# Performance work log

Measured on AMD Instinct MI355X. Metric: run time of the kernel, lower is better.

## Reference

```python
import jax, jax.numpy as jnp
import numpy as np

N = 100000   # num_nodes
R = 8        # num_relations
D = 64       # hidden_dim
E = 3200000  # num_edges


def setup_inputs() -> dict:
    key = jax.random.key(0)
    ks = jax.random.split(key, 10)
    s = 1.0 / np.sqrt(D)
    return {
        "x": jnp.arange(N, dtype=jnp.int64),
        "edge_index": jax.random.randint(ks[0], (2, E), 0, N, dtype=jnp.int64),
        "edge_type": jax.random.randint(ks[1], (E,), 0, R, dtype=jnp.int64),
        "emb": jax.random.normal(ks[2], (N, D), dtype=jnp.float32),
        "W1": jax.random.normal(ks[3], (R, D, D), dtype=jnp.float32) * s,
        "root1": jax.random.normal(ks[4], (D, D), dtype=jnp.float32) * s,
        "b1": jnp.zeros((D,), dtype=jnp.float32),
        "W2": jax.random.normal(ks[5], (R, D, D), dtype=jnp.float32) * s,
        "root2": jax.random.normal(ks[6], (D, D), dtype=jnp.float32) * s,
        "b2": jnp.zeros((D,), dtype=jnp.float32),
    }


def rgcn_conv(h, W, root, b, src, dst, etype):
    # per-edge gather of source features: [E, D]
    msgs = h[src]
    # composite segment id: (dst, relation) -> dst * R + relation
    seg = dst * R + etype
    sums = jax.ops.segment_sum(msgs, seg, num_segments=N * R)          # [N*R, D]
    cnt = jax.ops.segment_sum(jnp.ones((msgs.shape[0],), h.dtype), seg,
                              num_segments=N * R)                       # [N*R]
    mean = sums / jnp.maximum(cnt, 1.0)[:, None]                        # per-relation mean aggr
    mean = mean.reshape(N, R, D)
    # relation-specific transform + root weight + bias
    return jnp.einsum('nrd,rde->ne', mean, W) + h @ root + b


def reference(x, edge_index, edge_type, emb, W1, root1, b1, W2, root2, b2):
    src, dst = edge_index[0], edge_index[1]
    h = emb[x]                                   # embedding lookup
    h = rgcn_conv(h, W1, root1, b1, src, dst, edge_type)
    h = jax.nn.relu(h)                           # dropout = identity (eval mode)
    h = rgcn_conv(h, W2, root2, b2, src, dst, edge_type)
    return h
```

## Files before the change

### kernel.cpp

```cpp
#include <hip/hip_runtime.h>

#define N_NODES 100000
#define R_REL   8
#define D_DIM   64
#define E_EDGES 3200000
#define NSEG    (N_NODES * R_REL)
#define NB      1563
#define SEG_PER_BKT 512
#define BKT_CAP 2560
#define P1_BLOCKS 1250
#define P1_CHUNK  2560
#define ESRC_CAP 1280

typedef __attribute__((ext_vector_type(8))) short short8;
typedef __attribute__((ext_vector_type(4))) float f32x4;
typedef __attribute__((ext_vector_type(2))) float f32x2;

__device__ __forceinline__ unsigned short f2bf(float f) {
    unsigned u = __float_as_uint(f);
    u += 0x7fffu + ((u >> 16) & 1u);
    return (unsigned short)(u >> 16);
}

__device__ __forceinline__ int epack(int s, int d, int r) {
    return (s << 9) | ((d & 63) << 3) | r;
}

__global__ void init_cursor_kernel(int* __restrict__ bkt_cursor) {
    int t = blockIdx.x * 256 + threadIdx.x;
    if (t <= NB) bkt_cursor[t] = t * BKT_CAP;
}

__global__ void __launch_bounds__(512)
p1_scatter_kernel(const int* __restrict__ src, const int* __restrict__ dst,
                  const int* __restrict__ et, int* __restrict__ bkt_cursor,
                  int* __restrict__ packed) {
    __shared__ int hist[NB];
    __shared__ int cur[NB];
    int t = threadIdx.x;
    for (int i = t; i < NB; i += 512) hist[i] = 0;
    __syncthreads();
    int base = blockIdx.x * P1_CHUNK;
    for (int i = t * 4; i < P1_CHUNK; i += 2048) {
        int4 d4 = *(const int4*)(dst + base + i);
        atomicAdd(&hist[d4.x >> 6], 1);
        atomicAdd(&hist[d4.y >> 6], 1);
        atomicAdd(&hist[d4.z >> 6], 1);
        atomicAdd(&hist[d4.w >> 6], 1);
    }
    __syncthreads();
    for (int i = t; i < NB; i += 512) {
        int c = hist[i];
        cur[i] = c ? atomicAdd(&bkt_cursor[i], c) : 0;
    }
    __syncthreads();
    for (int i = t * 4; i < P1_CHUNK; i += 2048) {
        int4 s4 = *(const int4*)(src + base + i);
        int4 d4 = *(const int4*)(dst + base + i);
        int4 t4 = *(const int4*)(et  + base + i);
        int p0 = atomicAdd(&cur[d4.x >> 6], 1); packed[p0] = epack(s4.x, d4.x, t4.x);
        int p1 = atomicAdd(&cur[d4.y >> 6], 1); packed[p1] = epack(s4.y, d4.y, t4.y);
        int p2 = atomicAdd(&cur[d4.z >> 6], 1); packed[p2] = epack(s4.z, d4.z, t4.z);
        int p3 = atomicAdd(&cur[d4.w >> 6], 1); packed[p3] = epack(s4.w, d4.w, t4.w);
    }
}

__global__ void __launch_bounds__(512)
p2_sort_kernel(const int* __restrict__ packed, const int* __restrict__ bkt_cursor,
               int* __restrict__ starts, int* __restrict__ ends, int* __restrict__ esrc) {
    __shared__ int spk[BKT_CAP];
    __shared__ int scur[SEG_PER_BKT];
    __shared__ int wsum[8];
    int b = blockIdx.x;
    int t = threadIdx.x;
    int ebase = b * BKT_CAP;
    int ecnt  = bkt_cursor[b] - ebase;
    int segbase = b * SEG_PER_BKT;
    int nseg = NSEG - segbase; if (nseg > SEG_PER_BKT) nseg = SEG_PER_BKT;
    scur[t] = 0;
    __syncthreads();
    for (int i = t; i < ecnt; i += 512) {
        int p = packed[ebase + i];
        spk[i] = p;
        atomicAdd(&scur[p & 511], 1);
    }
    __syncthreads();
    int v = scur[t];
    int lane = t & 63, wid = t >> 6;
    int x = v;
#pragma unroll
    for (int off = 1; off < 64; off <<= 1) {
        int y = __shfl_up(x, off, 64);
        if (lane >= off) x += y;
    }
    if (lane == 63) wsum[wid] = x;
    __syncthreads();
    int woff = 0;
#pragma unroll
    for (int k = 0; k < 8; ++k) woff += (k < wid) ? wsum[k] : 0;
    int excl = x + woff - v;
    scur[t] = excl;
    if (t < nseg) starts[segbase + t] = ebase + excl;
    __syncthreads();
    for (int i = t; i < ecnt; i += 512) {
        int p = spk[i];
        int r = atomicAdd(&scur[p & 511], 1);
        esrc[ebase + r] = p >> 9;
    }
    __syncthreads();
    if (t < nseg) ends[segbase + t] = ebase + scur[t];
}

__global__ void __launch_bounds__(256)
prep_kernel(const float* __restrict__ W1, const float* __restrict__ root1,
            const float* __restrict__ W2, const float* __restrict__ root2,
            const float* __restrict__ emb,
            unsigned short* __restrict__ wbuf1, unsigned short* __restrict__ wbuf2,
            unsigned short* __restrict__ embb) {
    int b = blockIdx.x;
    if (b < 18) {
        int r = (b < 9) ? b : b - 9;
        const float* W    = (b < 9) ? W1 : W2;
        const float* root = (b < 9) ? root1 : root2;
        unsigned short* wbuf = (b < 9) ? wbuf1 : wbuf2;
        const float* src = (r < 8) ? (W + (size_t)r * 4096) : root;
        __shared__ float t[64][65];
        int a = threadIdx.x >> 2, c = threadIdx.x & 3;
#pragma unroll
        for (int i = 0; i < 4; ++i) {
            float4 v = *(const float4*)(src + a * 64 + c * 16 + i * 4);
            t[a][c * 16 + i * 4 + 0] = v.x;
            t[a][c * 16 + i * 4 + 1] = v.y;
            t[a][c * 16 + i * 4 + 2] = v.z;
            t[a][c * 16 + i * 4 + 3] = v.w;
        }
        __syncthreads();
        unsigned short* outrow = wbuf + (size_t)r * 4096 + a * 64;
#pragma unroll
        for (int i = 0; i < 4; ++i) {
            int k0 = c * 16 + i * 4;
            ushort4 o;
            o.x = f2bf(t[k0 + 0][a]); o.y = f2bf(t[k0 + 1][a]);
            o.z = f2bf(t[k0 + 2][a]); o.w = f2bf(t[k0 + 3][a]);
            *(ushort4*)(outrow + k0) = o;
        }
    } else {
        size_t base = ((size_t)(b - 18) * 256 + threadIdx.x) * 8;
        float4 v0 = *(const float4*)(emb + base);
        float4 v1 = *(const float4*)(emb + base + 4);
        uint4 o;
        o.x = f2bf(v0.x) | ((unsigned)f2bf(v0.y) << 16);
        o.y = f2bf(v0.z) | ((unsigned)f2bf(v0.w) << 16);
        o.z = f2bf(v1.x) | ((unsigned)f2bf(v1.y) << 16);
        o.w = f2bf(v1.z) | ((unsigned)f2bf(v1.w) << 16);
        *(uint4*)(embb + base) = o;
    }
}

__global__ void __launch_bounds__(512, 8)
fused_kernel(const unsigned short* __restrict__ hb, const int* __restrict__ esrc,
             const int* __restrict__ starts, const int* __restrict__ ends,
             const unsigned short* __restrict__ wbuf, const float* __restrict__ bias,
             void* __restrict__ out, int mode) {
    __shared__ unsigned short As[8][32][64];
    __shared__ int esrc_lds[ESRC_CAP];
    int tid = threadIdx.x;
    int g   = tid >> 4;
    int ml  = tid & 15;
    int n0  = blockIdx.x * 32;
    int sblk = n0 * R_REL;

    int E0 = starts[sblk];
    int L  = ends[sblk + 255] - E0;
    for (int i = tid; i < L; i += 512) esrc_lds[i] = esrc[E0 + i];
    __syncthreads();

    {
        int segb = sblk + g * R_REL;
        int4 eA = *(const int4*)(ends + segb);
        int4 eB = *(const int4*)(ends + segb + 4);
        int beg_cur = starts[segb] - E0;
        eA.x -= E0; eA.y -= E0; eA.z -= E0; eA.w -= E0;
        eB.x -= E0; eB.y -= E0; eB.z -= E0; eB.w -= E0;
        int end_cur = eA.x;
        int eN = eB.w;
        int r = 0;
        f32x2 a01 = {0.f, 0.f}, a23 = {0.f, 0.f};
        unsigned swz = (unsigned)((g & 7) << 4);

#define FLUSH()                                                          \
    do {                                                                 \
        float inv = __builtin_amdgcn_rcpf(                               \
            fmaxf((float)(end_cur - beg_cur), 1.0f));                    \
        ushort4 o;                                                       \
        o.x = f2bf(a01.x * inv); o.y = f2bf(a01.y * inv);                \
        o.z = f2bf(a23.x * inv); o.w = f2bf(a23.y * inv);                \
        *(ushort4*)((char*)As +                                          \
            ((unsigned)((r * 32 + g) * 128 + ml * 8) ^ swz)) = o;        \
        a01 = (f32x2){0.f, 0.f}; a23 = (f32x2){0.f, 0.f};                \
        ++r;                                                             \
        beg_cur = end_cur;                                               \
        end_cur = (r == 1) ? eA.y : (r == 2) ? eA.z : (r == 3) ? eA.w :  \
                  (r == 4) ? eB.x : (r == 5) ? eB.y : (r == 6) ? eB.z :  \
                  (r == 7) ? eB.w : 0x7fffffff;                          \
    } while (0)

        int e = beg_cur;
        while (e < eN) {
            int m = eN - e; if (m > 8) m = 8;
            uint2 rows[8];
#pragma unroll
            for (int i = 0; i < 8; ++i) {
                int ee = e + i; ee = (ee < eN) ? ee : (eN - 1);
                int sid = esrc_lds[ee];
                rows[i] = *(const uint2*)(hb + (size_t)sid * D_DIM + ml * 4);
            }
#pragma unroll
            for (int i = 0; i < 8; ++i) {
                if (i < m) {
                    while (e + i >= end_cur) FLUSH();
                    f32x2 u, v;
                    u.x = __uint_as_float(rows[i].x << 16);
                    u.y = __uint_as_float(rows[i].x & 0xffff0000u);
                    v.x = __uint_as_float(rows[i].y << 16);
                    v.y = __uint_as_float(rows[i].y & 0xffff0000u);
                    a01 += u;
                    a23 += v;
                }
            }
            e += m;
        }
        while (r < 8) FLUSH();
#undef FLUSH
    }

    int w  = tid >> 6;
    int kg = g & 3;
    int h  = w & 1;
    int q  = w >> 1;

    const unsigned short* rp = hb + (size_t)(n0 + h * 16 + ml) * D_DIM + kg * 8;
    short8 RA0 = *(const short8*)(rp);
    short8 RA1 = *(const short8*)(rp + 32);

    __syncthreads();

    int arow = h * 16 + ml;
    unsigned asw = (unsigned)((arow & 7) << 4);
    const char* asb = (const char*)As;

    f32x4 acc = {0, 0, 0, 0};
#pragma unroll 1
    for (int p = 0; p < 8; ++p) {
        unsigned base = (unsigned)((p * 32 + arow) * 128);
        short8 A0 = *(const short8*)(asb + ((base + kg * 16) ^ asw));
        short8 A1 = *(const short8*)(asb + ((base + 64 + kg * 16) ^ asw));
        const unsigned short* bp = wbuf + (size_t)p * 4096 + (q * 16 + ml) * 64 + kg * 8;
        short8 B0 = *(const short8*)(bp);
        short8 B1 = *(const short8*)(bp + 32);
        acc = __builtin_amdgcn_mfma_f32_16x16x32_bf16(A0, B0, acc, 0, 0, 0);
        acc = __builtin_amdgcn_mfma_f32_16x16x32_bf16(A1, B1, acc, 0, 0, 0);
    }
    {
        const unsigned short* bp = wbuf + (size_t)8 * 4096 + (q * 16 + ml) * 64 + kg * 8;
        short8 B0 = *(const short8*)(bp);
        short8 B1 = *(const short8*)(bp + 32);
        acc = __builtin_amdgcn_mfma_f32_16x16x32_bf16(RA0, B0, acc, 0, 0, 0);
        acc = __builtin_amdgcn_mfma_f32_16x16x32_bf16(RA1, B1, acc, 0, 0, 0);
    }

    float bv = bias[q * 16 + ml];
#pragma unroll
    for (int rg = 0; rg < 4; ++rg) {
        int node = n0 + h * 16 + kg * 4 + rg;
        float v = acc[rg] + bv;
        if (mode) {
            v = fmaxf(v, 0.f);
            ((unsigned short*)out)[(size_t)node * D_DIM + q * 16 + ml] = f2bf(v);
        } else {
            ((float*)out)[(size_t)node * D_DIM + q * 16 + ml] = v;
        }
    }
}


extern "C" void kernel_launch(void* const* d_in, const int* in_sizes, int n_in,
                              void* d_out, int out_size, void* d_ws, size_t ws_size,
                              hipStream_t stream) {
    const int*   ei    = (const int*)d_in[1];
    const int*   src   = ei;
    const int*   dst   = ei + E_EDGES;
    const int*   et    = (const int*)d_in[2];
    const float* emb   = (const float*)d_in[3];
    const float* W1    = (const float*)d_in[4];
    const float* root1 = (const float*)d_in[5];
    const float* b1    = (const float*)d_in[6];
    const float* W2    = (const float*)d_in[7];
    const float* root2 = (const float*)d_in[8];
    const float* b2    = (const float*)d_in[9];
    float*       out   = (float*)d_out;

    unsigned short* embb   = (unsigned short*)d_ws;
    unsigned short* h1b    = embb + (size_t)N_NODES * D_DIM;
    unsigned short* wbuf1  = h1b + (size_t)N_NODES * D_DIM;
    unsigned short* wbuf2  = wbuf1 + 9 * 4096;
    int*            starts = (int*)(wbuf2 + 9 * 4096);
    int*            ends   = starts + NSEG;
    int*            packed = ends + NSEG;
    int*            esrc   = packed + (size_t)NB * BKT_CAP;
    int*            bkt_cursor = esrc + (size_t)NB * BKT_CAP;

    init_cursor_kernel<<<7, 256, 0, stream>>>(bkt_cursor);
    p1_scatter_kernel <<<P1_BLOCKS, 512, 0, stream>>>(src, dst, et, bkt_cursor, packed);
    p2_sort_kernel    <<<NB, 512, 0, stream>>>(packed, bkt_cursor, starts, ends, esrc);

    prep_kernel<<<18 + (N_NODES * D_DIM) / 2048, 256, 0, stream>>>(
        W1, root1, W2, root2, emb, wbuf1, wbuf2, embb);

    const int blocks = N_NODES / 32;

    fused_kernel<<<blocks, 512, 0, stream>>>(embb, esrc, starts, ends, wbuf1, b1, h1b, 1);
    fused_kernel<<<blocks, 512, 0, stream>>>(h1b, esrc, starts, ends, wbuf2, b2, out, 0);
}
```

Baseline: 421.6 us.

## Use coarser 256-node buckets and split per-bucket sort across four blocks

Edge buckets grow from 64 to 256 destination nodes (2048 segments), so there are fewer buckets and the scatter pass needs fewer global cursor atomics and a smaller histogram. The sort pass runs four blocks per bucket. Each block re-reads the whole bucket from global memory to build counts and a prefix scan, then scatters only its quarter of the segments. The point is fewer, larger buckets and less per-block shared memory. The cost is redundant reads of each bucket and scalar rather than vectorized loads in the scatter pass.

Result: no change. 418.2 us (-0.8%).

```diff
diff --git a/kernel.cpp b/kernel.cpp
--- a/kernel.cpp
+++ b/kernel.cpp
@@ -5,11 +5,11 @@
 #define D_DIM   64
 #define E_EDGES 3200000
 #define NSEG    (N_NODES * R_REL)
-#define NB      1563
-#define SEG_PER_BKT 512
-#define BKT_CAP 2560
-#define P1_BLOCKS 1250
-#define P1_CHUNK  2560
+#define NB      391
+#define SEG_PER_BKT 2048
+#define BKT_CAP 9000
+#define P1_BLOCKS 512
+#define P1_CHUNK  (E_EDGES / P1_BLOCKS)
 #define ESRC_CAP 1280
 
 typedef __attribute__((ext_vector_type(8))) short short8;
@@ -23,7 +23,7 @@
 }
 
 __device__ __forceinline__ int epack(int s, int d, int r) {
-    return (s << 9) | ((d & 63) << 3) | r;
+    return (s << 11) | ((d & 255) << 3) | r;
 }
 
 __global__ void init_cursor_kernel(int* __restrict__ bkt_cursor) {
@@ -31,63 +31,55 @@
     if (t <= NB) bkt_cursor[t] = t * BKT_CAP;
 }
 
-__global__ void __launch_bounds__(512)
+__global__ void __launch_bounds__(256)
 p1_scatter_kernel(const int* __restrict__ src, const int* __restrict__ dst,
                   const int* __restrict__ et, int* __restrict__ bkt_cursor,
                   int* __restrict__ packed) {
     __shared__ int hist[NB];
     __shared__ int cur[NB];
     int t = threadIdx.x;
-    for (int i = t; i < NB; i += 512) hist[i] = 0;
+    for (int i = t; i < NB; i += 256) hist[i] = 0;
     __syncthreads();
     int base = blockIdx.x * P1_CHUNK;
-    for (int i = t * 4; i < P1_CHUNK; i += 2048) {
-        int4 d4 = *(const int4*)(dst + base + i);
-        atomicAdd(&hist[d4.x >> 6], 1);
-        atomicAdd(&hist[d4.y >> 6], 1);
-        atomicAdd(&hist[d4.z >> 6], 1);
-        atomicAdd(&hist[d4.w >> 6], 1);
-    }
-    __syncthreads();
-    for (int i = t; i < NB; i += 512) {
+    for (int i = t; i < P1_CHUNK; i += 256)
+        atomicAdd(&hist[dst[base + i] >> 8], 1);
+    __syncthreads();
+    for (int i = t; i < NB; i += 256) {
         int c = hist[i];
         cur[i] = c ? atomicAdd(&bkt_cursor[i], c) : 0;
     }
     __syncthreads();
-    for (int i = t * 4; i < P1_CHUNK; i += 2048) {
-        int4 s4 = *(const int4*)(src + base + i);
-        int4 d4 = *(const int4*)(dst + base + i);
-        int4 t4 = *(const int4*)(et  + base + i);
-        int p0 = atomicAdd(&cur[d4.x >> 6], 1); packed[p0] = epack(s4.x, d4.x, t4.x);
-        int p1 = atomicAdd(&cur[d4.y >> 6], 1); packed[p1] = epack(s4.y, d4.y, t4.y);
-        int p2 = atomicAdd(&cur[d4.z >> 6], 1); packed[p2] = epack(s4.z, d4.z, t4.z);
-        int p3 = atomicAdd(&cur[d4.w >> 6], 1); packed[p3] = epack(s4.w, d4.w, t4.w);
-    }
-}
-
-__global__ void __launch_bounds__(512)
+    for (int i = t; i < P1_CHUNK; i += 256) {
+        int e = base + i;
+        int d = dst[e];
+        int pos = atomicAdd(&cur[d >> 8], 1);
+        packed[pos] = epack(src[e], d, et[e]);
+    }
+}
+
+__global__ void __launch_bounds__(256)
 p2_sort_kernel(const int* __restrict__ packed, const int* __restrict__ bkt_cursor,
                int* __restrict__ starts, int* __restrict__ ends, int* __restrict__ esrc) {
-    __shared__ int spk[BKT_CAP];
     __shared__ int scur[SEG_PER_BKT];
-    __shared__ int wsum[8];
-    int b = blockIdx.x;
-    int t = threadIdx.x;
+    __shared__ int wsum[4];
+    int blk = blockIdx.x;
+    int b  = blk >> 2, qq = blk & 3;
+    int t  = threadIdx.x;
     int ebase = b * BKT_CAP;
-    int ecnt  = bkt_cursor[b] - ebase;
+    int eend  = bkt_cursor[b];
     int segbase = b * SEG_PER_BKT;
-    int nseg = NSEG - segbase; if (nseg > SEG_PER_BKT) nseg = SEG_PER_BKT;
-    scur[t] = 0;
-    __syncthreads();
-    for (int i = t; i < ecnt; i += 512) {
-        int p = packed[ebase + i];
-        spk[i] = p;
-        atomicAdd(&scur[p & 511], 1);
-    }
-    __syncthreads();
-    int v = scur[t];
+#pragma unroll
+    for (int i = 0; i < 8; ++i) scur[t + i * 256] = 0;
+    __syncthreads();
+    for (int e = ebase + t; e < eend; e += 256)
+        atomicAdd(&scur[packed[e] & 2047], 1);
+    __syncthreads();
+    int loc[8], s = 0;
+    int b8 = t * 8;
+#pragma unroll
+    for (int i = 0; i < 8; ++i) { loc[i] = scur[b8 + i]; s += loc[i]; }
     int lane = t & 63, wid = t >> 6;
-    int x = v;
+    int x = s;
 #pragma unroll
     for (int off = 1; off < 64; off <<= 1) {
         int y = __shfl_up(x, off, 64);
@@ -97,18 +89,31 @@
     __syncthreads();
     int woff = 0;
 #pragma unroll
-    for (int k = 0; k < 8; ++k) woff += (k < wid) ? wsum[k] : 0;
-    int excl = x + woff - v;
-    scur[t] = excl;
-    if (t < nseg) starts[segbase + t] = ebase + excl;
-    __syncthreads();
-    for (int i = t; i < ecnt; i += 512) {
-        int p = spk[i];
-        int r = atomicAdd(&scur[p & 511], 1);
-        esrc[ebase + r] = p >> 9;
-    }
-    __syncthreads();
-    if (t < nseg) ends[segbase + t] = ebase + scur[t];
+    for (int k = 0; k < 4; ++k) woff += (k < wid) ? wsum[k] : 0;
+    int run = x + woff - s;
+#pragma unroll
+    for (int i = 0; i < 8; ++i) { scur[b8 + i] = run; run += loc[i]; }
+    __syncthreads();
+#pragma unroll
+    for (int j = 0; j < 2; ++j) {
+        int ls = qq * 512 + j * 256 + t;
+        if (segbase + ls < NSEG) starts[segbase + ls] = ebase + scur[ls];
+    }
+    __syncthreads();
+    for (int e = ebase + t; e < eend; e += 256) {
+        int p = packed[e];
+        int ls = p & 2047;
+        if ((ls >> 9) == qq) {
+            int r = atomicAdd(&scur[ls], 1);
+            esrc[ebase + r] = p >> 11;
+        }
+    }
+    __syncthreads();
+#pragma unroll
+    for (int j = 0; j < 2; ++j) {
+        int ls = qq * 512 + j * 256 + t;
+        if (segbase + ls < NSEG) ends[segbase + ls] = ebase + scur[ls];
+    }
 }
 
 __global__ void __launch_bounds__(256)
@@ -310,9 +315,9 @@
     int*            esrc   = packed + (size_t)NB * BKT_CAP;
     int*            bkt_cursor = esrc + (size_t)NB * BKT_CAP;
 
-    init_cursor_kernel<<<7, 256, 0, stream>>>(bkt_cursor);
-    p1_scatter_kernel <<<P1_BLOCKS, 512, 0, stream>>>(src, dst, et, bkt_cursor, packed);
-    p2_sort_kernel    <<<NB, 512, 0, stream>>>(packed, bkt_cursor, starts, ends, esrc);
+    init_cursor_kernel<<<2, 256, 0, stream>>>(bkt_cursor);
+    p1_scatter_kernel <<<P1_BLOCKS, 256, 0, stream>>>(src, dst, et, bkt_cursor, packed);
+    p2_sort_kernel    <<<NB * 4, 256, 0, stream>>>(packed, bkt_cursor, starts, ends, esrc);
 
     prep_kernel<<<18 + (N_NODES * D_DIM) / 2048, 256, 0, stream>>>(
         W1, root1, W2, root2, emb, wbuf1, wbuf2, embb);
```
